# Optimization experiments

Measured on AMD Instinct MI355X. Metric: run time of the kernel, lower is better.

## Reference

```python
import jax, jax.numpy as jnp
import numpy as np

NDIM = 7  # window side; N = 49
NUM_HEADS = 12

def _rel_pos_index(ndim=NDIM):
    coords = np.stack(np.meshgrid(np.arange(ndim), np.arange(ndim), indexing='ij'))  # [2,7,7]
    cf = coords.reshape(2, -1)                      # [2,49]
    rel = cf[:, :, None] - cf[:, None, :]           # [2,49,49]
    rel = rel.transpose(1, 2, 0).copy()             # [49,49,2]
    rel[:, :, 0] += ndim - 1
    rel[:, :, 1] += ndim - 1
    rel[:, :, 0] *= 2 * ndim - 1
    return jnp.asarray(rel.sum(-1), dtype=jnp.int32)  # [49,49]

def setup_inputs() -> dict:
    key = jax.random.key(0)
    ks = jax.random.split(key, 6)
    B, N, C = 1024, NDIM * NDIM, 768
    x = jax.random.normal(ks[0], (B, N, C), dtype=jnp.float32)
    prev = jax.random.normal(ks[1], (B, NUM_HEADS, N, N), dtype=jnp.float32)
    # weights stored as [in, out] so forward is x @ W (matches torch Linear math)
    qkv_w = jax.random.normal(ks[2], (C, 3 * C), dtype=jnp.float32) * 0.02
    proj_w = jax.random.normal(ks[3], (C, C), dtype=jnp.float32) * 0.02
    proj_b = jax.random.normal(ks[4], (C,), dtype=jnp.float32) * 0.02
    bias_table = jax.random.normal(ks[5], ((2 * NDIM - 1) ** 2, NUM_HEADS), dtype=jnp.float32) * 0.02
    rel_idx = _rel_pos_index()
    return {"x": x, "prev": prev, "qkv_w": qkv_w, "proj_w": proj_w,
            "proj_b": proj_b, "bias_table": bias_table, "rel_idx": rel_idx}

def reference(x, prev, qkv_w, proj_w, proj_b, bias_table, rel_idx):
    B, N, C = x.shape
    H = NUM_HEADS
    hd = C // H
    scale = hd ** -0.5
    qkv = (x @ qkv_w).reshape(B, N, 3, H, hd)
    q = qkv[:, :, 0].transpose(0, 2, 1, 3)  # [B,H,N,hd]
    k = qkv[:, :, 1].transpose(0, 2, 1, 3)
    v = qkv[:, :, 2].transpose(0, 2, 1, 3)
    attn_score = jnp.einsum('bhnd,bhmd->bhnm', q, k) * scale  # [B,H,N,N]
    bias = bias_table[rel_idx.reshape(-1)].reshape(N, N, H).transpose(2, 0, 1)  # [H,N,N]
    attn_score = attn_score + bias[None]
    attn_score = attn_score + prev          # res_score=True path
    prev_out = attn_score
    attn = jax.nn.softmax(attn_score, axis=-1)
    out = jnp.einsum('bhnm,bhmd->bhnd', attn, v).transpose(0, 2, 1, 3).reshape(B, N, C)
    out = out @ proj_w + proj_b
    return (out, prev_out)
```

## Files before the change

kernel.cpp:

```cpp
#include <hip/hip_runtime.h>

typedef unsigned short u16;
typedef unsigned int u32;
typedef float f32x4 __attribute__((ext_vector_type(4)));
typedef __bf16 bf16x8 __attribute__((ext_vector_type(8)));

#define DEV static __device__ __forceinline__

DEV u16 f2bf(float f) {
  u32 u = __builtin_bit_cast(u32, f);
  u += 0x7fffu + ((u >> 16) & 1u);
  return (u16)(u >> 16);
}

DEV float bf2f(u16 v) {
  u32 u = ((u32)v) << 16;
  return __builtin_bit_cast(float, u);
}

DEV void gload_lds16(const void* g, void* l) {
  __builtin_amdgcn_global_load_lds(
      (const __attribute__((address_space(1))) u32*)g,
      (__attribute__((address_space(3))) u32*)l, 16, 0, 0);
}


__global__ __launch_bounds__(256) void cvt_bf16(const float* __restrict__ in,
                                                u16* __restrict__ out, int n4) {
  int i = blockIdx.x * 256 + threadIdx.x;
  const int stride = gridDim.x * 256;
  for (; i < n4; i += stride) {
    const float4 v = ((const float4*)in)[i];
    ushort4 o;
    o.x = f2bf(v.x); o.y = f2bf(v.y); o.z = f2bf(v.z); o.w = f2bf(v.w);
    ((ushort4*)out)[i] = o;
  }
}

__global__ __launch_bounds__(256) void cvtT_bf16(const float* __restrict__ in,
                                                 u16* __restrict__ out, int K, int N) {
  int i = blockIdx.x * 256 + threadIdx.x;
  if (i >= N * K) return;
  int n = i / K, k = i - n * K;
  out[i] = f2bf(in[(long)k * N + n]);
}

__global__ __launch_bounds__(256) void bias_pre(const float* __restrict__ bias_table,
                                                const int* __restrict__ rel_idx,
                                                float* __restrict__ biasM) {
  int i = blockIdx.x * 256 + threadIdx.x;
  if (i >= 12 * 2401) return;
  int h = i / 2401, p = i - h * 2401;
  biasM[i] = bias_table[rel_idx[p] * 12 + h];
}

template <bool OUT_BF16>
__global__ __launch_bounds__(512, 2) void gemm256(
    const u16* __restrict__ A, const u16* __restrict__ BT,
    void* __restrict__ C, const float* __restrict__ bias,
    int M, int N, int K, int nbn) {
  __shared__ alignas(16) char lds[131072];
  const int t = threadIdx.x;
  const int w = t >> 6, l = t & 63, lr = l & 15, lhi = l >> 4;
  const int wr = w >> 2, wc = w & 3;

  const int nwg = gridDim.x;
  const int q = nwg >> 3, r = nwg & 7;
  const int xcd = blockIdx.x & 7, lid = blockIdx.x >> 3;
  const int swz = (xcd < r ? xcd * (q + 1) : r * (q + 1) + (xcd - r) * q) + lid;
  const int bm = swz / nbn, bn = swz % nbn;

  const int T = K >> 5;
  const long Kb = (long)K * 2;

  const int unswz = (l & 7) ^ (l >> 3);
  const int arow = 2 * (l >> 3) + (unswz >> 2);
  const int acolb = (unswz & 3) << 4;
  const char* gA0 = (const char*)A + (long)(bm * 256 + w * 32 + arow) * Kb + acolb;
  const char* gA1 = gA0 + 16 * Kb;
  const char* gB0 = (const char*)BT + (long)(bn * 256 + w * 32 + arow) * Kb + acolb;
  const char* gB1 = gB0 + 16 * Kb;
  const int ldA0 = w * 2048, ldA1 = w * 2048 + 1024;
  const int ldB0 = 16384 + w * 2048, ldB1 = 16384 + w * 2048 + 1024;

#define STAGE(tt)                               \
  {                                             \
    const int bb = ((tt) & 3) * 32768;          \
    const long ko = (long)(tt) * 64;            \
    gload_lds16(gA0 + ko, lds + bb + ldA0);     \
    gload_lds16(gA1 + ko, lds + bb + ldA1);     \
    gload_lds16(gB0 + ko, lds + bb + ldB0);     \
    gload_lds16(gB1 + ko, lds + bb + ldB1);     \
  }
#define BAR                                  \
  asm volatile("" ::: "memory");             \
  __builtin_amdgcn_s_barrier();              \
  asm volatile("" ::: "memory")

  const int rblk = ((((lr & 1) << 2) | lhi) ^ (lr >> 1));
  const int aoff0 = (wr * 64 + (lr >> 1)) * 128 + rblk * 16;
  const int boff0 = 16384 + (wc * 32 + (lr >> 1)) * 128 + rblk * 16;

  f32x4 acc[8][4];
#pragma unroll
  for (int m = 0; m < 8; ++m)
#pragma unroll
    for (int n = 0; n < 4; ++n) acc[m][n] = (f32x4){0.f, 0.f, 0.f, 0.f};
  bf16x8 afrX[4], bfrX[4], afrY[4], bfrY[4];

#define CLUSTER1(S)                                                        \
  __builtin_amdgcn_s_setprio(1);                                           \
  _Pragma("unroll") for (int m = 0; m < 4; ++m)                            \
      _Pragma("unroll") for (int n = 0; n < 4; ++n)                        \
          acc[m][n] = __builtin_amdgcn_mfma_f32_16x16x32_bf16(             \
              afr##S[m], bfr##S[n], acc[m][n], 0, 0, 0);                   \
  __builtin_amdgcn_s_setprio(0)
#define CLUSTER2(S)                                                        \
  __builtin_amdgcn_s_setprio(1);                                           \
  _Pragma("unroll") for (int m = 0; m < 4; ++m)                            \
      _Pragma("unroll") for (int n = 0; n < 4; ++n)                        \
          acc[m + 4][n] = __builtin_amdgcn_mfma_f32_16x16x32_bf16(         \
              afr2[m], bfr##S[n], acc[m + 4][n], 0, 0, 0);                 \
  __builtin_amdgcn_s_setprio(0)

#define BODY(kt, S, R)                                                     \
  {                                                                        \
    if ((kt) + 3 < T) STAGE((kt) + 3);                                     \
    const int bbc = ((kt) & 3) * 32768;                                    \
    const int nx = ((kt) + 1 < T) ? (kt) + 1 : (kt);                       \
    const int bbn = (nx & 3) * 32768;                                      \
    bf16x8 afr2[4];                                                        \
    _Pragma("unroll") for (int m = 0; m < 4; ++m)                          \
        afr2[m] = *(const bf16x8*)(lds + bbc + aoff0 + (m + 4) * 1024);    \
    CLUSTER1(S);                                                           \
    _Pragma("unroll") for (int n = 0; n < 4; ++n)                          \
        bfr##R[n] = *(const bf16x8*)(lds + bbn + boff0 + n * 1024);        \
    CLUSTER2(S);                                                           \
    _Pragma("unroll") for (int m = 0; m < 4; ++m)                          \
        afr##R[m] = *(const bf16x8*)(lds + bbn + aoff0 + m * 1024);        \
    if ((kt) + 3 < T) {                                                    \
      asm volatile("s_waitcnt vmcnt(4)" ::: "memory");                     \
    } else {                                                               \
      asm volatile("s_waitcnt vmcnt(0)" ::: "memory");                     \
    }                                                                      \
    BAR;                                                                   \
  }

  STAGE(0); STAGE(1); STAGE(2);
  asm volatile("s_waitcnt vmcnt(4)" ::: "memory");
  BAR;
#pragma unroll
  for (int n = 0; n < 4; ++n) bfrX[n] = *(const bf16x8*)(lds + boff0 + n * 1024);
#pragma unroll
  for (int m = 0; m < 4; ++m) afrX[m] = *(const bf16x8*)(lds + aoff0 + m * 1024);

  for (int i = 0; i < T / 2; ++i) {
    BODY(2 * i, X, Y);
    BODY(2 * i + 1, Y, X);
  }
#undef STAGE
#undef BAR
#undef CLUSTER1
#undef CLUSTER2
#undef BODY

  const int row0 = bm * 256 + wr * 128 + 4 * lhi;
  const int col0 = bn * 256 + wc * 64 + lr;
  if (OUT_BF16) {
    u16* Cc = (u16*)C;
#pragma unroll
    for (int m = 0; m < 8; ++m)
#pragma unroll
      for (int rr = 0; rr < 4; ++rr) {
        const long row = row0 + m * 16 + rr;
#pragma unroll
        for (int n = 0; n < 4; ++n)
          Cc[row * N + col0 + n * 16] = f2bf(acc[m][n][rr]);
      }
  } else {
    float* Cf = (float*)C;
    float bv[4];
#pragma unroll
    for (int n = 0; n < 4; ++n) bv[n] = bias[col0 + n * 16];
#pragma unroll
    for (int m = 0; m < 8; ++m)
#pragma unroll
      for (int rr = 0; rr < 4; ++rr) {
        const long row = row0 + m * 16 + rr;
#pragma unroll
        for (int n = 0; n < 4; ++n)
          Cf[row * N + col0 + n * 16] = acc[m][n][rr] + bv[n];
      }
  }
}

__global__ __launch_bounds__(256) void attn_kernel(
    const u16* __restrict__ qkv,
    const float* __restrict__ prev,
    const float* __restrict__ biasM,
    float* __restrict__ prev_out,
    u16* __restrict__ attn_out) {
  __shared__ u16 Qs[64][72];
  __shared__ u16 Ks[64][72];
  __shared__ u16 VTs[64][72];
  __shared__ u16 SB[2432];

  const int bh = blockIdx.x;
  const int b = bh / 12, h = bh % 12;
  const int t = threadIdx.x, w = t >> 6, l = t & 63, lr = l & 15, lhi = l >> 4;

  const u16* base = qkv + (long)(b * 49) * 2304 + h * 64;
  for (int idx = t; idx < 49 * 16; idx += 256) {
    const int n = idx >> 4, c4 = (idx & 15) << 2;
    const u16* rp = base + (long)n * 2304;
    ushort4 qv = *(const ushort4*)(rp + c4);
    ushort4 kv = *(const ushort4*)(rp + 768 + c4);
    ushort4 vv = *(const ushort4*)(rp + 1536 + c4);
    *(ushort4*)&Qs[n][c4] = qv;
    *(ushort4*)&Ks[n][c4] = kv;
    VTs[c4 + 0][n] = vv.x;
    VTs[c4 + 1][n] = vv.y;
    VTs[c4 + 2][n] = vv.z;
    VTs[c4 + 3][n] = vv.w;
  }
  for (int idx = t; idx < 1024; idx += 256) {
    const int j = idx & 15;
    if (j) VTs[idx >> 4][48 + j] = 0;
  }

  float prevR[10], biasR[10];
  {
    const float* pv = prev + (long)bh * 2401;
    const float* bm = biasM + h * 2401;
#pragma unroll
    for (int k = 0; k < 10; ++k) {
      const int i = t + 256 * k;
      if (i < 2401) {
        prevR[k] = pv[i];
        biasR[k] = bm[i];
      }
    }
  }

  asm volatile("s_waitcnt lgkmcnt(0)" ::: "memory");
  __builtin_amdgcn_s_barrier();
  asm volatile("" ::: "memory");

  bf16x8 af0 = *(const bf16x8*)&Qs[16 * w + lr][lhi * 8];
  bf16x8 af1 = *(const bf16x8*)&Qs[16 * w + lr][32 + lhi * 8];
  f32x4 sacc[4];
#pragma unroll
  for (int tc = 0; tc < 4; ++tc) {
    sacc[tc] = (f32x4){0.f, 0.f, 0.f, 0.f};
    bf16x8 b0 = *(const bf16x8*)&Ks[16 * tc + lr][lhi * 8];
    bf16x8 b1 = *(const bf16x8*)&Ks[16 * tc + lr][32 + lhi * 8];
    sacc[tc] = __builtin_amdgcn_mfma_f32_16x16x32_bf16(af0, b0, sacc[tc], 0, 0, 0);
    sacc[tc] = __builtin_amdgcn_mfma_f32_16x16x32_bf16(af1, b1, sacc[tc], 0, 0, 0);
  }

  asm volatile("s_waitcnt vmcnt(0)" ::: "memory");
#pragma unroll
  for (int k = 0; k < 10; ++k) {
    const int i = t + 256 * k;
    if (i < 2401) SB[i] = f2bf(prevR[k] + biasR[k]);
  }
  asm volatile("s_waitcnt lgkmcnt(0)" ::: "memory");
  __builtin_amdgcn_s_barrier();
  asm volatile("" ::: "memory");

  u16 (*Ps)[72] = Qs;
  const int nrow0 = 16 * w + 4 * lhi;
  float rs[4];
#pragma unroll
  for (int r = 0; r < 4; ++r) {
    const int row = nrow0 + r;
    const bool rv = row < 49;
    float sv[4];
#pragma unroll
    for (int tc = 0; tc < 4; ++tc) {
      const int col = 16 * tc + lr;
      const bool valid = rv && (col < 49);
      const int sidx = (row < 49 ? row : 48) * 49 + (col < 49 ? col : 48);
      const float pb = bf2f(SB[sidx]);
      const float s = sacc[tc][r] * 0.125f + pb;
      if (valid) SB[sidx] = f2bf(s);
      sv[tc] = valid ? s : -INFINITY;
    }
    float mx = fmaxf(fmaxf(sv[0], sv[1]), fmaxf(sv[2], sv[3]));
#pragma unroll
    for (int off = 8; off; off >>= 1) mx = fmaxf(mx, __shfl_xor(mx, off, 16));
    float e[4], sum = 0.f;
#pragma unroll
    for (int tc = 0; tc < 4; ++tc) {
      e[tc] = __expf(sv[tc] - mx);
      sum += e[tc];
    }
#pragma unroll
    for (int off = 8; off; off >>= 1) sum += __shfl_xor(sum, off, 16);
    rs[r] = 1.0f / sum;
#pragma unroll
    for (int tc = 0; tc < 4; ++tc)
      Ps[row][16 * tc + lr] = rv ? f2bf(e[tc]) : (u16)0;
  }
  __syncthreads();

  bf16x8 pf0 = *(const bf16x8*)&Ps[16 * w + lr][lhi * 8];
  bf16x8 pf1 = *(const bf16x8*)&Ps[16 * w + lr][32 + lhi * 8];
  f32x4 oacc[4];
#pragma unroll
  for (int dc = 0; dc < 4; ++dc) {
    oacc[dc] = (f32x4){0.f, 0.f, 0.f, 0.f};
    bf16x8 v0 = *(const bf16x8*)&VTs[16 * dc + lr][lhi * 8];
    bf16x8 v1 = *(const bf16x8*)&VTs[16 * dc + lr][32 + lhi * 8];
    oacc[dc] = __builtin_amdgcn_mfma_f32_16x16x32_bf16(pf0, v0, oacc[dc], 0, 0, 0);
    oacc[dc] = __builtin_amdgcn_mfma_f32_16x16x32_bf16(pf1, v1, oacc[dc], 0, 0, 0);
  }

#pragma unroll
  for (int r = 0; r < 4; ++r) {
    const int row = nrow0 + r;
    if (row < 49) {
#pragma unroll
      for (int dc = 0; dc < 4; ++dc)
        Ks[row][16 * dc + lr] = f2bf(oacc[dc][r] * rs[r]);
    }
  }
  __syncthreads();

  {
    u16* ob = attn_out + (long)(b * 49) * 768 + h * 64;
    for (int idx = t; idx < 49 * 8; idx += 256) {
      const int row = idx >> 3, cc = (idx & 7) << 3;
      *(ulonglong2*)&ob[(long)row * 768 + cc] = *(const ulonglong2*)&Ks[row][cc];
    }
    float* pout = prev_out + (long)bh * 2401;
    for (int i = t; i < 2401; i += 256) pout[i] = bf2f(SB[i]);
  }
}

extern "C" void kernel_launch(void* const* d_in, const int* in_sizes, int n_in,
                              void* d_out, int out_size, void* d_ws, size_t ws_size,
                              hipStream_t stream) {
  const float* x = (const float*)d_in[0];
  const float* prev = (const float*)d_in[1];
  const float* qkv_w = (const float*)d_in[2];
  const float* proj_w = (const float*)d_in[3];
  const float* proj_b = (const float*)d_in[4];
  const float* bias_table = (const float*)d_in[5];
  const int* rel_idx = (const int*)d_in[6];

  const int B = in_sizes[0] / (49 * 768);
  const int M = B * 49;

  float* out0 = (float*)d_out;
  float* out1 = out0 + (size_t)M * 768;

  char* ws = (char*)d_ws;
  u16* xbf = (u16*)ws;
  u16* qkvbf = (u16*)(ws + (size_t)M * 768 * 2);
  u16* qkvwT = (u16*)(ws + (size_t)M * 768 * 2 + (size_t)M * 2304 * 2);
  u16* projwT = qkvwT + 2304 * 768;
  float* biasM = (float*)(projwT + 768 * 768);

  bias_pre<<<(12 * 2401 + 255) / 256, 256, 0, stream>>>(bias_table, rel_idx, biasM);
  cvt_bf16<<<2048, 256, 0, stream>>>(x, xbf, M * 768 / 4);
  cvtT_bf16<<<(2304 * 768 + 255) / 256, 256, 0, stream>>>(qkv_w, qkvwT, 768, 2304);
  cvtT_bf16<<<(768 * 768 + 255) / 256, 256, 0, stream>>>(proj_w, projwT, 768, 768);

  gemm256<true><<<(M / 256) * (2304 / 256), 512, 0, stream>>>(
      xbf, qkvwT, qkvbf, nullptr, M, 2304, 768, 2304 / 256);

  attn_kernel<<<B * 12, 256, 0, stream>>>(qkvbf, prev, biasM, out1, xbf);

  gemm256<false><<<(M / 256) * (768 / 256), 512, 0, stream>>>(
      xbf, projwT, out0, proj_b, M, 768, 768, 768 / 256);
}
```

Before: 475.7 us.

## Deepen GEMM LDS pipeline to five stages and tile weight transposes

The bf16 GEMM's LDS buffer ring grows from four to five 32KB stages, using 160KB of LDS. Global-to-LDS prefetch now runs four k-steps ahead, tracked by a rotating buffer offset with adjusted vmcnt waits, to hide more memory latency. The weight transpose-convert kernels now stage 32x32 tiles in shared memory, so both reads and writes are coalesced instead of strided. The risks are that the larger LDS footprint limits occupancy to one workgroup per CU, and that the ring-offset logic must stay in sync with the wait counts.

```diff
diff --git a/kernel.cpp b/kernel.cpp
--- a/kernel.cpp
+++ b/kernel.cpp
@@ -37,12 +37,24 @@
   }
 }
 
-__global__ __launch_bounds__(256) void cvtT_bf16(const float* __restrict__ in,
+__global__ __launch_bounds__(256) void cvtT_tile(const float* __restrict__ in,
                                                  u16* __restrict__ out, int K, int N) {
-  int i = blockIdx.x * 256 + threadIdx.x;
-  if (i >= N * K) return;
-  int n = i / K, k = i - n * K;
-  out[i] = f2bf(in[(long)k * N + n]);
+  __shared__ float tile[32][33];
+  const int nbx = N >> 5;
+  const int bx = blockIdx.x % nbx, by = blockIdx.x / nbx;
+  const int tx = threadIdx.x & 31, ty = threadIdx.x >> 5;
+  const int gcol = bx * 32 + tx;
+#pragma unroll
+  for (int j = 0; j < 4; ++j) {
+    const int r = ty + 8 * j;
+    tile[r][tx] = in[(long)(by * 32 + r) * N + gcol];
+  }
+  __syncthreads();
+#pragma unroll
+  for (int j = 0; j < 4; ++j) {
+    const int r = ty + 8 * j;
+    out[(long)(bx * 32 + r) * K + by * 32 + tx] = f2bf(tile[tx][r]);
+  }
 }
 
 __global__ __launch_bounds__(256) void bias_pre(const float* __restrict__ bias_table,
@@ -59,7 +71,7 @@
     const u16* __restrict__ A, const u16* __restrict__ BT,
     void* __restrict__ C, const float* __restrict__ bias,
     int M, int N, int K, int nbn) {
-  __shared__ alignas(16) char lds[131072];
+  __shared__ alignas(16) char lds[163840];
   const int t = threadIdx.x;
   const int w = t >> 6, l = t & 63, lr = l & 15, lhi = l >> 4;
   const int wr = w >> 2, wc = w & 3;
@@ -83,14 +95,13 @@
   const int ldA0 = w * 2048, ldA1 = w * 2048 + 1024;
   const int ldB0 = 16384 + w * 2048, ldB1 = 16384 + w * 2048 + 1024;
 
-#define STAGE(tt)                               \
+#define STAGE(tt, bb)                           \
   {                                             \
-    const int bb = ((tt) & 3) * 32768;          \
     const long ko = (long)(tt) * 64;            \
-    gload_lds16(gA0 + ko, lds + bb + ldA0);     \
-    gload_lds16(gA1 + ko, lds + bb + ldA1);     \
-    gload_lds16(gB0 + ko, lds + bb + ldB0);     \
-    gload_lds16(gB1 + ko, lds + bb + ldB1);     \
+    gload_lds16(gA0 + ko, lds + (bb) + ldA0);   \
+    gload_lds16(gA1 + ko, lds + (bb) + ldA1);   \
+    gload_lds16(gB0 + ko, lds + (bb) + ldB0);   \
+    gload_lds16(gB1 + ko, lds + (bb) + ldB1);   \
   }
 #define BAR                                  \
   asm volatile("" ::: "memory");             \
@@ -125,30 +136,34 @@
 
 #define BODY(kt, S, R)                                                     \
   {                                                                        \
-    if ((kt) + 3 < T) STAGE((kt) + 3);                                     \
-    const int bbc = ((kt) & 3) * 32768;                                    \
-    const int nx = ((kt) + 1 < T) ? (kt) + 1 : (kt);                       \
-    const int bbn = (nx & 3) * 32768;                                      \
+    int sbb = bb0 - 32768; if (sbb < 0) sbb = 131072;       \
+    int nbb = bb0 + 32768; if (nbb > 131072) nbb = 0;       \
+    if ((kt) + 4 < T) STAGE((kt) + 4, sbb);                                \
     bf16x8 afr2[4];                                                        \
     _Pragma("unroll") for (int m = 0; m < 4; ++m)                          \
-        afr2[m] = *(const bf16x8*)(lds + bbc + aoff0 + (m + 4) * 1024);    \
+        afr2[m] = *(const bf16x8*)(lds + bb0 + aoff0 + (m + 4) * 1024);    \
     CLUSTER1(S);                                                           \
+    const int rb = ((kt) + 1 < T) ? nbb : bb0;                             \
     _Pragma("unroll") for (int n = 0; n < 4; ++n)                          \
-        bfr##R[n] = *(const bf16x8*)(lds + bbn + boff0 + n * 1024);        \
+        bfr##R[n] = *(const bf16x8*)(lds + rb + boff0 + n * 1024);         \
     CLUSTER2(S);                                                           \
     _Pragma("unroll") for (int m = 0; m < 4; ++m)                          \
-        afr##R[m] = *(const bf16x8*)(lds + bbn + aoff0 + m * 1024);        \
-    if ((kt) + 3 < T) {                                                    \
+        afr##R[m] = *(const bf16x8*)(lds + rb + aoff0 + m * 1024);         \
+    if ((kt) + 4 < T) {                                                    \
+      asm volatile("s_waitcnt vmcnt(8)" ::: "memory");                     \
+    } else if ((kt) + 3 < T) {                                             \
       asm volatile("s_waitcnt vmcnt(4)" ::: "memory");                     \
     } else {                                                               \
       asm volatile("s_waitcnt vmcnt(0)" ::: "memory");                     \
     }                                                                      \
     BAR;                                                                   \
-  }
-
-  STAGE(0); STAGE(1); STAGE(2);
-  asm volatile("s_waitcnt vmcnt(4)" ::: "memory");
+    bb0 = nbb;                                                             \
+  }
+
+  STAGE(0, 0); STAGE(1, 32768); STAGE(2, 65536); STAGE(3, 98304);
+  asm volatile("s_waitcnt vmcnt(8)" ::: "memory");
   BAR;
+  int bb0 = 0;
 #pragma unroll
   for (int n = 0; n < 4; ++n) bfrX[n] = *(const bf16x8*)(lds + boff0 + n * 1024);
 #pragma unroll
@@ -364,8 +379,8 @@
 
   bias_pre<<<(12 * 2401 + 255) / 256, 256, 0, stream>>>(bias_table, rel_idx, biasM);
   cvt_bf16<<<2048, 256, 0, stream>>>(x, xbf, M * 768 / 4);
-  cvtT_bf16<<<(2304 * 768 + 255) / 256, 256, 0, stream>>>(qkv_w, qkvwT, 768, 2304);
-  cvtT_bf16<<<(768 * 768 + 255) / 256, 256, 0, stream>>>(proj_w, projwT, 768, 768);
+  cvtT_tile<<<(2304 / 32) * (768 / 32), 256, 0, stream>>>(qkv_w, qkvwT, 768, 2304);
+  cvtT_tile<<<(768 / 32) * (768 / 32), 256, 0, stream>>>(proj_w, projwT, 768, 768);
 
   gemm256<true><<<(M / 256) * (2304 / 256), 512, 0, stream>>>(
       xbf, qkvwT, qkvbf, nullptr, M, 2304, 768, 2304 / 256);
```

Result: no change. 471.1 us (-1.0%).

## Fuse prep kernels with tiled transpose and use wave-local sync in attention

Applied to the files above, without the earlier changes.

Merges the bias gather, the x conversion and both weight transpose-conversions into one launch. The weight transposes now go through a padded 32x33 LDS tile so global reads and writes are coalesced, instead of the strided per-element reads used before. In the attention kernel, the two block-wide barriers become wave-local LDS waits, and each wave writes back only its own 16 rows of output and prev_out. This is correct only if every wave reads solely LDS rows it wrote itself, so it carries a race risk if that ownership assumption fails.

```diff
diff --git a/kernel.cpp b/kernel.cpp
--- a/kernel.cpp
+++ b/kernel.cpp
@@ -24,34 +24,45 @@
       (__attribute__((address_space(3))) u32*)l, 16, 0, 0);
 }
 
-
-__global__ __launch_bounds__(256) void cvt_bf16(const float* __restrict__ in,
-                                                u16* __restrict__ out, int n4) {
-  int i = blockIdx.x * 256 + threadIdx.x;
-  const int stride = gridDim.x * 256;
-  for (; i < n4; i += stride) {
-    const float4 v = ((const float4*)in)[i];
-    ushort4 o;
-    o.x = f2bf(v.x); o.y = f2bf(v.y); o.z = f2bf(v.z); o.w = f2bf(v.w);
-    ((ushort4*)out)[i] = o;
-  }
-}
-
-__global__ __launch_bounds__(256) void cvtT_bf16(const float* __restrict__ in,
-                                                 u16* __restrict__ out, int K, int N) {
-  int i = blockIdx.x * 256 + threadIdx.x;
-  if (i >= N * K) return;
-  int n = i / K, k = i - n * K;
-  out[i] = f2bf(in[(long)k * N + n]);
-}
-
-__global__ __launch_bounds__(256) void bias_pre(const float* __restrict__ bias_table,
-                                                const int* __restrict__ rel_idx,
-                                                float* __restrict__ biasM) {
-  int i = blockIdx.x * 256 + threadIdx.x;
-  if (i >= 12 * 2401) return;
-  int h = i / 2401, p = i - h * 2401;
-  biasM[i] = bias_table[rel_idx[p] * 12 + h];
+__global__ __launch_bounds__(256) void prep(
+    const float* __restrict__ x, u16* __restrict__ xbf, int n4,
+    const float* __restrict__ qkv_w, u16* __restrict__ qkvwT,
+    const float* __restrict__ proj_w, u16* __restrict__ projwT,
+    const float* __restrict__ bias_table, const int* __restrict__ rel_idx,
+    float* __restrict__ biasM) {
+  __shared__ float tile[32][33];
+  const int bid = blockIdx.x;
+  if (bid < 2048) {
+    int i = bid * 256 + threadIdx.x;
+    for (; i < n4; i += 2048 * 256) {
+      const float4 v = ((const float4*)x)[i];
+      ushort4 o;
+      o.x = f2bf(v.x); o.y = f2bf(v.y); o.z = f2bf(v.z); o.w = f2bf(v.w);
+      ((ushort4*)xbf)[i] = o;
+    }
+  } else if (bid < 2048 + 1728 + 576) {
+    const bool qk = bid < 2048 + 1728;
+    const int b2 = qk ? bid - 2048 : bid - (2048 + 1728);
+    const float* in = qk ? qkv_w : proj_w;
+    u16* out = qk ? qkvwT : projwT;
+    const int N = qk ? 2304 : 768;
+    const int nbx = N >> 5;
+    const int bx = b2 % nbx, by = b2 / nbx;
+    const int tx = threadIdx.x & 31, ty = threadIdx.x >> 5;
+#pragma unroll
+    for (int j = 0; j < 4; ++j)
+      tile[ty + 8 * j][tx] = in[(long)(by * 32 + ty + 8 * j) * N + bx * 32 + tx];
+    __syncthreads();
+#pragma unroll
+    for (int j = 0; j < 4; ++j)
+      out[(long)(bx * 32 + ty + 8 * j) * 768 + by * 32 + tx] = f2bf(tile[tx][ty + 8 * j]);
+  } else {
+    const int i = (bid - (2048 + 1728 + 576)) * 256 + threadIdx.x;
+    if (i < 12 * 2401) {
+      const int h = i / 2401, p = i - h * 2401;
+      biasM[i] = bias_table[rel_idx[p] * 12 + h];
+    }
+  }
 }
 
 template <bool OUT_BF16>
@@ -302,7 +313,9 @@
     for (int tc = 0; tc < 4; ++tc)
       Ps[row][16 * tc + lr] = rv ? f2bf(e[tc]) : (u16)0;
   }
-  __syncthreads();
+
+  asm volatile("s_waitcnt lgkmcnt(0)" ::: "memory");
+  __builtin_amdgcn_sched_barrier(0);
 
   bf16x8 pf0 = *(const bf16x8*)&Ps[16 * w + lr][lhi * 8];
   bf16x8 pf1 = *(const bf16x8*)&Ps[16 * w + lr][32 + lhi * 8];
@@ -322,19 +335,22 @@
     if (row < 49) {
 #pragma unroll
       for (int dc = 0; dc < 4; ++dc)
-        Ks[row][16 * dc + lr] = f2bf(oacc[dc][r] * rs[r]);
-    }
-  }
-  __syncthreads();
+        Ps[row][16 * dc + lr] = f2bf(oacc[dc][r] * rs[r]);
+    }
+  }
+  asm volatile("s_waitcnt lgkmcnt(0)" ::: "memory");
+  __builtin_amdgcn_sched_barrier(0);
 
   {
+    const int r0 = 16 * w;
+    const int r1 = (16 * w + 16 < 49) ? 16 * w + 16 : 49;
     u16* ob = attn_out + (long)(b * 49) * 768 + h * 64;
-    for (int idx = t; idx < 49 * 8; idx += 256) {
-      const int row = idx >> 3, cc = (idx & 7) << 3;
-      *(ulonglong2*)&ob[(long)row * 768 + cc] = *(const ulonglong2*)&Ks[row][cc];
+    for (int it = l; it < (r1 - r0) * 8; it += 64) {
+      const int row = r0 + (it >> 3), cc = (it & 7) << 3;
+      *(ulonglong2*)&ob[(long)row * 768 + cc] = *(const ulonglong2*)&Ps[row][cc];
     }
     float* pout = prev_out + (long)bh * 2401;
-    for (int i = t; i < 2401; i += 256) pout[i] = bf2f(SB[i]);
+    for (int i = r0 * 49 + l; i < r1 * 49; i += 64) pout[i] = bf2f(SB[i]);
   }
 }
 
@@ -362,10 +378,9 @@
   u16* projwT = qkvwT + 2304 * 768;
   float* biasM = (float*)(projwT + 768 * 768);
 
-  bias_pre<<<(12 * 2401 + 255) / 256, 256, 0, stream>>>(bias_table, rel_idx, biasM);
-  cvt_bf16<<<2048, 256, 0, stream>>>(x, xbf, M * 768 / 4);
-  cvtT_bf16<<<(2304 * 768 + 255) / 256, 256, 0, stream>>>(qkv_w, qkvwT, 768, 2304);
-  cvtT_bf16<<<(768 * 768 + 255) / 256, 256, 0, stream>>>(proj_w, projwT, 768, 768);
+  prep<<<2048 + 1728 + 576 + 113, 256, 0, stream>>>(
+      x, xbf, M * 768 / 4, qkv_w, qkvwT, proj_w, projwT,
+      bias_table, rel_idx, biasM);
 
   gemm256<true><<<(M / 256) * (2304 / 256), 512, 0, stream>>>(
       xbf, qkvwT, qkvbf, nullptr, M, 2304, 768, 2304 / 256);
```

Result: faster. 455.9 us (-4.2%).
